# Kernel tuning notes

Hardware: AMD Instinct MI355X
Metric: run time of the kernel (lower is better)

## Reference

```python
import jax, jax.numpy as jnp
import numpy as np

H = 8  # num_heads

def setup_inputs() -> dict:
    key = jax.random.key(0)
    ks = jax.random.split(key, 10)
    B, N, C = 2048, 50, 256
    x = jax.random.normal(ks[0], (B, N, C), dtype=jnp.float32)
    adj = jax.random.uniform(ks[1], (B, N, N), dtype=jnp.float32)
    matrix = jax.random.normal(ks[2], (B, N, N), dtype=jnp.float32)
    s = 0.02
    Wq = jax.random.normal(ks[3], (C, C), dtype=jnp.float32) * s
    bq = jnp.zeros((C,), dtype=jnp.float32)
    Wk = jax.random.normal(ks[4], (C, C), dtype=jnp.float32) * s
    bk = jnp.zeros((C,), dtype=jnp.float32)
    Wa = jax.random.normal(ks[5], (N * H, N), dtype=jnp.float32) * s
    ba = jnp.zeros((N * H,), dtype=jnp.float32)
    Wm = jax.random.normal(ks[6], (N * H, N), dtype=jnp.float32) * s
    bm = jnp.zeros((N * H,), dtype=jnp.float32)
    lambdas = jnp.tile(jnp.array([[1.0, 0.0, 0.0]], dtype=jnp.float32), (H, 1))
    return {"x": x, "adj": adj, "matrix": matrix, "Wq": Wq, "bq": bq,
            "Wk": Wk, "bk": bk, "Wa": Wa, "ba": ba, "Wm": Wm, "bm": bm,
            "lambdas": lambdas}

def reference(x, adj, matrix, Wq, bq, Wk, bk, Wa, ba, Wm, bm, lambdas):
    B, N, C = x.shape
    D = C // H
    # torch Linear: y = x @ W.T + b
    q = (jnp.einsum('bnc,dc->bnd', x, Wq) + bq).reshape(B, N, H, D).transpose(0, 2, 1, 3)
    k = (jnp.einsum('bnc,dc->bnd', x, Wk) + bk).reshape(B, N, H, D).transpose(0, 2, 1, 3)
    # NOTE: original code computes v with self.k (faithful to source)
    v = k
    # scale uses full dim C (x.shape[-1]), not head_dim, as in source
    attn = jax.nn.softmax(jnp.einsum('bhnd,bhmd->bhnm', q, k) * (C ** -0.5), axis=-1)
    adj_a = jax.nn.softmax(
        (jnp.einsum('bnm,km->bnk', adj, Wa) + ba).reshape(B, N, H, N).transpose(0, 2, 1, 3), axis=-1)
    mat_a = jax.nn.softmax(
        (jnp.einsum('bnm,km->bnk', matrix, Wm) + bm).reshape(B, N, H, N).transpose(0, 2, 1, 3), axis=-1)
    lam = jax.nn.softmax(lambdas, axis=-1)  # [H, 3]
    l0 = lam[:, 0][None, :, None, None]
    l1 = lam[:, 1][None, :, None, None]
    l2 = lam[:, 2][None, :, None, None]
    mix = l0 * attn + l1 * adj_a + l2 * mat_a  # [B, H, N, N]
    out = jnp.einsum('bhnm,bhmd->bhnd', mix, v).transpose(0, 2, 1, 3).reshape(B, N, C)
    return out
```

## Files before the change

kernel.cpp:

```cpp
#include <hip/hip_runtime.h>
#include <stdint.h>


typedef __attribute__((ext_vector_type(8))) short short8;
typedef __attribute__((ext_vector_type(4))) float f32x4;
typedef unsigned short u16;

#define L2E 1.4426950408889634f

__device__ __forceinline__ u16 f2bf(float f) {
  unsigned int u = __float_as_uint(f);
  u = (u + 0x7FFFu + ((u >> 16) & 1u)) >> 16;
  return (u16)u;
}
__device__ __forceinline__ unsigned cvt_pk_bf16(float a, float b) {
  unsigned r;
  asm("v_cvt_pk_bf16_f32 %0, %1, %2" : "=v"(r) : "v"(a), "v"(b));
  return r;
}
__device__ __forceinline__ float exp2_fast(float x) {
#if __has_builtin(__builtin_amdgcn_exp2f)
  return __builtin_amdgcn_exp2f(x);
#else
  return __expf(x * 0.6931471805599453f);
#endif
}
__device__ __forceinline__ void lds_fence() {
  asm volatile("s_waitcnt lgkmcnt(0)" ::: "memory");
}

__global__ __launch_bounds__(256) void cast_all(
    const float* __restrict__ adj, const float* __restrict__ mat,
    const float* __restrict__ Wq, const float* __restrict__ Wk,
    const float* __restrict__ Wa, const float* __restrict__ Wm,
    u16* __restrict__ da, u16* __restrict__ dm, u16* __restrict__ wqk,
    u16* __restrict__ wab, u16* __restrict__ wmb,
    u16* __restrict__ qws, u16* __restrict__ kws) {
  const int blk = blockIdx.x, tid = threadIdx.x;
  if (blk < 2048) {
    const int total8 = (102416 * 64) / 8;
    for (int i8 = blk * 256 + tid; i8 < total8; i8 += 2048 * 256) {
      int r = i8 >> 3, c = (i8 & 7) * 8;
      short8 oa = (short8){0,0,0,0,0,0,0,0};
      short8 om = (short8){0,0,0,0,0,0,0,0};
      if (r < 102400) {
        size_t base = (size_t)r * 50;
#pragma unroll
        for (int p = 0; p < 4; ++p) {
          int col = c + 2 * p;
          if (col < 50) {
            float2 va = *(const float2*)(adj + base + col);
            float2 vm = *(const float2*)(mat + base + col);
            oa[2*p] = f2bf(va.x); oa[2*p+1] = f2bf(va.y);
            om[2*p] = f2bf(vm.x); om[2*p+1] = f2bf(vm.y);
          }
        }
      }
      *(short8*)(da + (size_t)i8 * 8) = oa;
      *(short8*)(dm + (size_t)i8 * 8) = om;
    }
  } else if (blk < 2112) {
    int idx8 = (blk - 2048) * 256 + tid;
    int r = idx8 >> 5, c = (idx8 & 31) * 8;
    const float* src = (r < 256) ? (Wq + (size_t)r * 256 + c)
                                 : (Wk + (size_t)(r - 256) * 256 + c);
    float4 v0 = *(const float4*)(src);
    float4 v1 = *(const float4*)(src + 4);
    short8 o;
    o[0] = f2bf(v0.x); o[1] = f2bf(v0.y); o[2] = f2bf(v0.z); o[3] = f2bf(v0.w);
    o[4] = f2bf(v1.x); o[5] = f2bf(v1.y); o[6] = f2bf(v1.z); o[7] = f2bf(v1.w);
    *(short8*)(wqk + (size_t)idx8 * 8) = o;
  } else if (blk < 2216) {
    int idx = (blk - 2112) * 256 + tid;
    int r = idx >> 6, c = idx & 63;
    float va = 0.f, vm = 0.f;
    if (r < 400 && c < 50) { va = Wa[r * 50 + c]; vm = Wm[r * 50 + c]; }
    wab[idx] = f2bf(va); wmb[idx] = f2bf(vm);
  } else {
    short8 z = (short8){0,0,0,0,0,0,0,0};
    *(short8*)(qws + (size_t)819200 * 32 + tid * 8) = z;
    *(short8*)(kws + (size_t)819200 * 32 + tid * 8) = z;
  }
}

__global__ __launch_bounds__(256) void proj_kernel(
    const float* __restrict__ x, const u16* __restrict__ wqk,
    const float* __restrict__ bq, const float* __restrict__ bk,
    u16* __restrict__ qws, u16* __restrict__ kws) {
  __shared__ char xa[64 * 512];
  __shared__ char wb[64 * 512];
  const int tid = threadIdx.x;
  const int m0 = blockIdx.x * 64;

#pragma unroll
  for (int t = 0; t < 16; ++t) {
    int idx = tid + t * 256;
    int r = idx >> 6, c4 = idx & 63;
    float4 v = *(const float4*)(x + (size_t)(m0 + r) * 256 + c4 * 4);
    unsigned long long pk = (unsigned long long)f2bf(v.x)
                          | ((unsigned long long)f2bf(v.y) << 16)
                          | ((unsigned long long)f2bf(v.z) << 32)
                          | ((unsigned long long)f2bf(v.w) << 48);
    int byte = (r * 512 + c4 * 8) ^ ((r & 7) << 4);
    *(unsigned long long*)(xa + byte) = pk;
  }
  __syncthreads();

  const int w = tid >> 6, l = tid & 63, lo = l & 15, g = l >> 4;
  short8 a[8];
  const int ra = 16 * w + lo;
#pragma unroll
  for (int ks = 0; ks < 8; ++ks)
    a[ks] = *(const short8*)(xa + ((ra * 512 + ks * 64 + g * 16) ^ ((ra & 7) << 4)));
  size_t mb[4];
#pragma unroll
  for (int i = 0; i < 4; ++i) {
    int m = m0 + 16 * w + 4 * g + i;
    int b = m / 50;
    int n = m - 50 * b;
    mb[i] = (size_t)b * 12800 + (size_t)n * 32;
  }

  for (int nt = 0; nt < 8; ++nt) {
    __syncthreads();
#pragma unroll
    for (int t = 0; t < 8; ++t) {
      int idx = tid + t * 256;
      int r = idx >> 5, c8 = idx & 31;
      short8 v = *(const short8*)(wqk + (size_t)(nt * 64 + r) * 256 + c8 * 8);
      int byte = (r * 512 + c8 * 16) ^ ((r & 7) << 4);
      *(short8*)(wb + byte) = v;
    }
    __syncthreads();

    f32x4 acc[4];
#pragma unroll
    for (int tj = 0; tj < 4; ++tj) acc[tj] = (f32x4){0.f, 0.f, 0.f, 0.f};
#pragma unroll
    for (int ks = 0; ks < 8; ++ks) {
#pragma unroll
      for (int tj = 0; tj < 4; ++tj) {
        int rb = 16 * tj + lo;
        short8 bb = *(const short8*)(wb + ((rb * 512 + ks * 64 + g * 16) ^ ((rb & 7) << 4)));
        acc[tj] = __builtin_amdgcn_mfma_f32_16x16x32_bf16(a[ks], bb, acc[tj], 0, 0, 0);
      }
    }
    const int n0 = nt * 64;
#pragma unroll
    for (int tj = 0; tj < 4; ++tj) {
      int j = n0 + 16 * tj + lo;
      int jj = j & 255;
      float bias = (j < 256) ? bq[jj] : bk[jj];
      u16* dst = (j < 256) ? qws : kws;
      int hh = jj >> 5, d = jj & 31;
#pragma unroll
      for (int i = 0; i < 4; ++i)
        dst[mb[i] + (size_t)hh * 1600 + d] = f2bf(acc[tj][i] + bias);
    }
  }
}

__device__ __forceinline__ void sm_pv_tile(
    f32x4 (&S)[4], const float (&bml)[4][4], float sl2e, float lam,
    u16* pb, const short8 (&vb)[2][2], f32x4 (&Otj)[2], int tj, int lo, int g) {
  float p[4][4];
#pragma unroll
  for (int ti = 0; ti < 4; ++ti)
#pragma unroll
    for (int i = 0; i < 4; ++i)
      p[ti][i] = exp2_fast(S[ti][i] * sl2e + bml[ti][i]);
  float t0 = (p[0][0] + p[0][1]) + (p[0][2] + p[0][3]);
  float t1 = (p[1][0] + p[1][1]) + (p[1][2] + p[1][3]);
  float t2 = (p[2][0] + p[2][1]) + (p[2][2] + p[2][3]);
  float t3 = (p[3][0] + p[3][1]) + (p[3][2] + p[3][3]);
  float sum = (t0 + t1) + (t2 + t3);
  sum += __shfl_xor(sum, 16);
  sum += __shfl_xor(sum, 32);
  float r = lam * __builtin_amdgcn_rcpf(sum);
  u16* base = pb + (tj & 1) * 1152 + lo * 72;
#pragma unroll
  for (int ti = 0; ti < 4; ++ti) {
    uint2 pk;
    pk.x = cvt_pk_bf16(p[ti][0] * r, p[ti][1] * r);
    pk.y = cvt_pk_bf16(p[ti][2] * r, p[ti][3] * r);
    *(uint2*)(base + 16 * ti + 4 * g) = pk;
  }
  lds_fence();
#pragma unroll
  for (int ks = 0; ks < 2; ++ks) {
    short8 pa = *(const short8*)(pb + (tj & 1) * 1152 + lo * 72 + ks * 32 + g * 8);
#pragma unroll
    for (int tjv = 0; tjv < 2; ++tjv)
      Otj[tjv] = __builtin_amdgcn_mfma_f32_16x16x32_bf16(pa, vb[tjv][ks], Otj[tjv], 0, 0, 0);
  }
}

__device__ __forceinline__ void adj_phase(
    const u16* __restrict__ aBase, const u16* __restrict__ bBase,
    const float* __restrict__ biasPtr, float lam,
    u16* pb, const short8 (&vb)[2][2], f32x4 (&O)[4][2], int lo, int g) {
  short8 af[4][2];
#pragma unroll
  for (int ti = 0; ti < 4; ++ti)
#pragma unroll
    for (int ks = 0; ks < 2; ++ks)
      af[ti][ks] = *(const short8*)(aBase + (size_t)(lo + 16 * ti) * 64 + ks * 32 + g * 8);
  float bml[4][4];
#pragma unroll
  for (int ti = 0; ti < 4; ++ti)
#pragma unroll
    for (int i = 0; i < 4; ++i) {
      int m = 16 * ti + 4 * g + i;
      bml[ti][i] = (m < 50) ? biasPtr[m] * L2E : -1.0e30f;
    }
#pragma unroll
  for (int tj = 0; tj < 4; ++tj) {
    short8 bf0 = *(const short8*)(bBase + (size_t)(lo + 16 * tj) * 64 + g * 8);
    short8 bf1 = *(const short8*)(bBase + (size_t)(lo + 16 * tj) * 64 + 32 + g * 8);
    f32x4 S[4];
#pragma unroll
    for (int ti = 0; ti < 4; ++ti) S[ti] = (f32x4){0.f, 0.f, 0.f, 0.f};
#pragma unroll
    for (int ti = 0; ti < 4; ++ti)
      S[ti] = __builtin_amdgcn_mfma_f32_16x16x32_bf16(af[ti][0], bf0, S[ti], 0, 0, 0);
#pragma unroll
    for (int ti = 0; ti < 4; ++ti)
      S[ti] = __builtin_amdgcn_mfma_f32_16x16x32_bf16(af[ti][1], bf1, S[ti], 0, 0, 0);
    sm_pv_tile(S, bml, L2E, lam, pb, vb, O[tj], tj, lo, g);
  }
}

__global__ __launch_bounds__(256) void attn_kernel(
    const u16* __restrict__ qws, const u16* __restrict__ kws,
    const u16* __restrict__ adjb, const u16* __restrict__ matb,
    const u16* __restrict__ wab, const u16* __restrict__ wmb,
    const float* __restrict__ ba, const float* __restrict__ bm,
    const float* __restrict__ lambdas, float* __restrict__ out) {
  __shared__ u16 smem[4][2304];
  const int tid = threadIdx.x;
  const int w = tid >> 6, l = tid & 63, lo = l & 15, g = l >> 4;
  const int bh = blockIdx.x * 4 + w;
  const int b = bh >> 3, h = bh & 7;
  u16* sh = smem[w];

  float la = lambdas[h * 3 + 0], lb = lambdas[h * 3 + 1], lc = lambdas[h * 3 + 2];
  float lmx = fmaxf(la, fmaxf(lb, lc));
  float e0 = __expf(la - lmx), e1 = __expf(lb - lmx), e2 = __expf(lc - lmx);
  float einv = 1.f / (e0 + e1 + e2);
  float lam0 = e0 * einv, lam1 = e1 * einv, lam2 = e2 * einv;

  {
    const u16* kr = kws + (size_t)bh * 1600 + (size_t)l * 32;
#pragma unroll
    for (int ch = 0; ch < 4; ++ch) {
      short8 v = (short8){0, 0, 0, 0, 0, 0, 0, 0};
      if (l < 50) v = *(const short8*)(kr + ch * 8);
#pragma unroll
      for (int jj = 0; jj < 8; ++jj)
        sh[(ch * 8 + jj) * 72 + l] = (u16)v[jj];
    }
  }
  lds_fence();
  short8 vb[2][2];
#pragma unroll
  for (int tjv = 0; tjv < 2; ++tjv)
#pragma unroll
    for (int ks = 0; ks < 2; ++ks)
      vb[tjv][ks] = *(const short8*)(sh + (lo + 16 * tjv) * 72 + ks * 32 + g * 8);

  f32x4 O[4][2];
#pragma unroll
  for (int ti = 0; ti < 4; ++ti)
#pragma unroll
    for (int tjv = 0; tjv < 2; ++tjv) O[ti][tjv] = (f32x4){0.f, 0.f, 0.f, 0.f};

  {
    short8 af[4];
#pragma unroll
    for (int ti = 0; ti < 4; ++ti)
      af[ti] = *(const short8*)(kws + (size_t)bh * 1600 + (size_t)(lo + 16 * ti) * 32 + g * 8);
    float bml[4][4];
#pragma unroll
    for (int ti = 0; ti < 4; ++ti)
#pragma unroll
      for (int i = 0; i < 4; ++i)
        bml[ti][i] = (16 * ti + 4 * g + i < 50) ? 0.f : -1.0e30f;
#pragma unroll
    for (int tj = 0; tj < 4; ++tj) {
      short8 qf = *(const short8*)(qws + (size_t)bh * 1600 + (size_t)(lo + 16 * tj) * 32 + g * 8);
      f32x4 S[4];
#pragma unroll
      for (int ti = 0; ti < 4; ++ti) S[ti] = (f32x4){0.f, 0.f, 0.f, 0.f};
#pragma unroll
      for (int ti = 0; ti < 4; ++ti)
        S[ti] = __builtin_amdgcn_mfma_f32_16x16x32_bf16(af[ti], qf, S[ti], 0, 0, 0);
      sm_pv_tile(S, bml, 0.0625f * L2E, lam0, sh, vb, O[tj], tj, lo, g);
    }
  }
  adj_phase(wab + (size_t)h * 3200, adjb + (size_t)b * 3200, ba + h * 50,
            lam1, sh, vb, O, lo, g);
  adj_phase(wmb + (size_t)h * 3200, matb + (size_t)b * 3200, bm + h * 50,
            lam2, sh, vb, O, lo, g);

  float* ob = out + ((size_t)b * 50) * 256 + h * 32;
#pragma unroll
  for (int ti = 0; ti < 4; ++ti)
#pragma unroll
    for (int i = 0; i < 4; ++i) {
      int n = 16 * ti + 4 * g + i;
      if (n < 50) {
#pragma unroll
        for (int tjv = 0; tjv < 2; ++tjv)
          ob[(size_t)n * 256 + 16 * tjv + lo] = O[ti][tjv][i];
      }
    }
}

extern "C" void kernel_launch(void* const* d_in, const int* in_sizes, int n_in,
                              void* d_out, int out_size, void* d_ws, size_t ws_size,
                              hipStream_t stream) {
  const float* x       = (const float*)d_in[0];
  const float* adj     = (const float*)d_in[1];
  const float* mat     = (const float*)d_in[2];
  const float* Wq      = (const float*)d_in[3];
  const float* bq      = (const float*)d_in[4];
  const float* Wk      = (const float*)d_in[5];
  const float* bk      = (const float*)d_in[6];
  const float* Wa      = (const float*)d_in[7];
  const float* ba      = (const float*)d_in[8];
  const float* Wm      = (const float*)d_in[9];
  const float* bm      = (const float*)d_in[10];
  const float* lambdas = (const float*)d_in[11];
  float* out = (float*)d_out;

  char* ws = (char*)d_ws;
  u16* wqk  = (u16*)ws; ws += (size_t)512 * 256 * 2;
  u16* wab  = (u16*)ws; ws += (size_t)416 * 64 * 2;
  u16* wmb  = (u16*)ws; ws += (size_t)416 * 64 * 2;
  u16* adjb = (u16*)ws; ws += (size_t)102416 * 64 * 2;
  u16* matb = (u16*)ws; ws += (size_t)102416 * 64 * 2;
  u16* qws  = (u16*)ws; ws += (size_t)819264 * 32 * 2;
  u16* kws  = (u16*)ws; ws += (size_t)819264 * 32 * 2;

  cast_all<<<2217, 256, 0, stream>>>(adj, mat, Wq, Wk, Wa, Wm,
                                     adjb, matb, wqk, wab, wmb, qws, kws);
  proj_kernel<<<1600, 256, 0, stream>>>(x, wqk, bq, bk, qws, kws);
  attn_kernel<<<4096, 256, 0, stream>>>(qws, kws, adjb, matb, wab, wmb, ba, bm, lambdas, out);
}
```

Before: 203.9 us.

## Fuse adj/matrix bf16 cast into attention kernel via swizzled LDS staging

```diff
diff --git a/kernel.cpp b/kernel.cpp
--- a/kernel.cpp
+++ b/kernel.cpp
@@ -26,41 +26,19 @@
 #endif
 }
 __device__ __forceinline__ void lds_fence() {
-  asm volatile("s_waitcnt lgkmcnt(0)" ::: "memory");
+  asm volatile("s_waitcnt lgkmcnt(0)");
 }
 
 __global__ __launch_bounds__(256) void cast_all(
-    const float* __restrict__ adj, const float* __restrict__ mat,
     const float* __restrict__ Wq, const float* __restrict__ Wk,
     const float* __restrict__ Wa, const float* __restrict__ Wm,
-    u16* __restrict__ da, u16* __restrict__ dm, u16* __restrict__ wqk,
-    u16* __restrict__ wab, u16* __restrict__ wmb,
+    const float* __restrict__ ba, const float* __restrict__ bm,
+    u16* __restrict__ wqk, u16* __restrict__ wab, u16* __restrict__ wmb,
+    float* __restrict__ bap, float* __restrict__ bmp,
     u16* __restrict__ qws, u16* __restrict__ kws) {
   const int blk = blockIdx.x, tid = threadIdx.x;
-  if (blk < 2048) {
-    const int total8 = (102416 * 64) / 8;
-    for (int i8 = blk * 256 + tid; i8 < total8; i8 += 2048 * 256) {
-      int r = i8 >> 3, c = (i8 & 7) * 8;
-      short8 oa = (short8){0,0,0,0,0,0,0,0};
-      short8 om = (short8){0,0,0,0,0,0,0,0};
-      if (r < 102400) {
-        size_t base = (size_t)r * 50;
-#pragma unroll
-        for (int p = 0; p < 4; ++p) {
-          int col = c + 2 * p;
-          if (col < 50) {
-            float2 va = *(const float2*)(adj + base + col);
-            float2 vm = *(const float2*)(mat + base + col);
-            oa[2*p] = f2bf(va.x); oa[2*p+1] = f2bf(va.y);
-            om[2*p] = f2bf(vm.x); om[2*p+1] = f2bf(vm.y);
-          }
-        }
-      }
-      *(short8*)(da + (size_t)i8 * 8) = oa;
-      *(short8*)(dm + (size_t)i8 * 8) = om;
-    }
-  } else if (blk < 2112) {
-    int idx8 = (blk - 2048) * 256 + tid;
+  if (blk < 64) {
+    int idx8 = blk * 256 + tid;
     int r = idx8 >> 5, c = (idx8 & 31) * 8;
     const float* src = (r < 256) ? (Wq + (size_t)r * 256 + c)
                                  : (Wk + (size_t)(r - 256) * 256 + c);
@@ -70,8 +48,8 @@
     o[0] = f2bf(v0.x); o[1] = f2bf(v0.y); o[2] = f2bf(v0.z); o[3] = f2bf(v0.w);
     o[4] = f2bf(v1.x); o[5] = f2bf(v1.y); o[6] = f2bf(v1.z); o[7] = f2bf(v1.w);
     *(short8*)(wqk + (size_t)idx8 * 8) = o;
-  } else if (blk < 2216) {
-    int idx = (blk - 2112) * 256 + tid;
+  } else if (blk < 168) {
+    int idx = (blk - 64) * 256 + tid;
     int r = idx >> 6, c = idx & 63;
     float va = 0.f, vm = 0.f;
     if (r < 400 && c < 50) { va = Wa[r * 50 + c]; vm = Wm[r * 50 + c]; }
@@ -80,6 +58,13 @@
     short8 z = (short8){0,0,0,0,0,0,0,0};
     *(short8*)(qws + (size_t)819200 * 32 + tid * 8) = z;
     *(short8*)(kws + (size_t)819200 * 32 + tid * 8) = z;
+#pragma unroll
+    for (int j = 0; j < 2; ++j) {
+      int idx = tid + 256 * j;
+      int hh = idx >> 6, m = idx & 63;
+      bap[idx] = (m < 50) ? ba[hh * 50 + m] : 0.f;
+      bmp[idx] = (m < 50) ? bm[hh * 50 + m] : 0.f;
+    }
   }
 }
 
@@ -158,6 +143,11 @@
         dst[mb[i] + (size_t)hh * 1600 + d] = f2bf(acc[tj][i] + bias);
     }
   }
+}
+
+__device__ __forceinline__ short8 ldsfrag(const u16* bLds, int row, int ks, int g) {
+  return *(const short8*)((const char*)bLds +
+         (((row) * 128 + ks * 64 + g * 16) ^ (((row) & 7) << 4)));
 }
 
 __device__ __forceinline__ void sm_pv_tile(
@@ -196,9 +186,8 @@
 }
 
 __device__ __forceinline__ void adj_phase(
-    const u16* __restrict__ aBase, const u16* __restrict__ bBase,
-    const float* __restrict__ biasPtr, float lam,
-    u16* pb, const short8 (&vb)[2][2], f32x4 (&O)[4][2], int lo, int g) {
+    const u16* __restrict__ aBase, const u16* bLds, const float* __restrict__ bPad,
+    float lam, u16* pb, const short8 (&vb)[2][2], f32x4 (&O)[4][2], int lo, int g) {
   short8 af[4][2];
 #pragma unroll
   for (int ti = 0; ti < 4; ++ti)
@@ -207,42 +196,70 @@
       af[ti][ks] = *(const short8*)(aBase + (size_t)(lo + 16 * ti) * 64 + ks * 32 + g * 8);
   float bml[4][4];
 #pragma unroll
-  for (int ti = 0; ti < 4; ++ti)
-#pragma unroll
-    for (int i = 0; i < 4; ++i) {
-      int m = 16 * ti + 4 * g + i;
-      bml[ti][i] = (m < 50) ? biasPtr[m] * L2E : -1.0e30f;
-    }
+  for (int ti = 0; ti < 4; ++ti) {
+    f32x4 bv = *(const f32x4*)(bPad + 16 * ti + 4 * g);
+#pragma unroll
+    for (int i = 0; i < 4; ++i)
+      bml[ti][i] = (16 * ti + 4 * g + i < 50) ? bv[i] * L2E : -1.0e30f;
+  }
+  short8 bc0 = ldsfrag(bLds, lo, 0, g);
+  short8 bc1 = ldsfrag(bLds, lo, 1, g);
 #pragma unroll
   for (int tj = 0; tj < 4; ++tj) {
-    short8 bf0 = *(const short8*)(bBase + (size_t)(lo + 16 * tj) * 64 + g * 8);
-    short8 bf1 = *(const short8*)(bBase + (size_t)(lo + 16 * tj) * 64 + 32 + g * 8);
+    short8 bn0, bn1;
+    if (tj < 3) {
+      bn0 = ldsfrag(bLds, lo + 16 * (tj + 1), 0, g);
+      bn1 = ldsfrag(bLds, lo + 16 * (tj + 1), 1, g);
+    }
     f32x4 S[4];
 #pragma unroll
     for (int ti = 0; ti < 4; ++ti) S[ti] = (f32x4){0.f, 0.f, 0.f, 0.f};
 #pragma unroll
     for (int ti = 0; ti < 4; ++ti)
-      S[ti] = __builtin_amdgcn_mfma_f32_16x16x32_bf16(af[ti][0], bf0, S[ti], 0, 0, 0);
+      S[ti] = __builtin_amdgcn_mfma_f32_16x16x32_bf16(af[ti][0], bc0, S[ti], 0, 0, 0);
 #pragma unroll
     for (int ti = 0; ti < 4; ++ti)
-      S[ti] = __builtin_amdgcn_mfma_f32_16x16x32_bf16(af[ti][1], bf1, S[ti], 0, 0, 0);
+      S[ti] = __builtin_amdgcn_mfma_f32_16x16x32_bf16(af[ti][1], bc1, S[ti], 0, 0, 0);
     sm_pv_tile(S, bml, L2E, lam, pb, vb, O[tj], tj, lo, g);
+    bc0 = bn0; bc1 = bn1;
   }
 }
 
 __global__ __launch_bounds__(256) void attn_kernel(
     const u16* __restrict__ qws, const u16* __restrict__ kws,
-    const u16* __restrict__ adjb, const u16* __restrict__ matb,
+    const float* __restrict__ adjf, const float* __restrict__ matf,
     const u16* __restrict__ wab, const u16* __restrict__ wmb,
-    const float* __restrict__ ba, const float* __restrict__ bm,
+    const float* __restrict__ bap, const float* __restrict__ bmp,
     const float* __restrict__ lambdas, float* __restrict__ out) {
   __shared__ u16 smem[4][2304];
+  __shared__ u16 adjm[2][4096];
   const int tid = threadIdx.x;
   const int w = tid >> 6, l = tid & 63, lo = l & 15, g = l >> 4;
   const int bh = blockIdx.x * 4 + w;
   const int b = bh >> 3, h = bh & 7;
   u16* sh = smem[w];
 
+  {
+    const float* s0 = adjf + (size_t)b * 2500;
+    const float* s1 = matf + (size_t)b * 2500;
+#pragma unroll
+    for (int mtx = 0; mtx < 2; ++mtx) {
+      const float* s = mtx ? s1 : s0;
+      unsigned* dstm = (unsigned*)adjm[mtx];
+#pragma unroll
+      for (int t = 0; t < 8; ++t) {
+        int word = tid + t * 256;
+        int r = word >> 5, c2 = word & 31;
+        unsigned val = 0;
+        if (r < 50 && c2 < 25) {
+          float2 v = *(const float2*)(s + r * 50 + c2 * 2);
+          val = cvt_pk_bf16(v.x, v.y);
+        }
+        dstm[word ^ ((r & 7) << 2)] = val;
+      }
+    }
+  }
+
   float la = lambdas[h * 3 + 0], lb = lambdas[h * 3 + 1], lc = lambdas[h * 3 + 2];
   float lmx = fmaxf(la, fmaxf(lb, lc));
   float e0 = __expf(la - lmx), e1 = __expf(lb - lmx), e2 = __expf(lc - lmx);
@@ -285,22 +302,26 @@
 #pragma unroll
       for (int i = 0; i < 4; ++i)
         bml[ti][i] = (16 * ti + 4 * g + i < 50) ? 0.f : -1.0e30f;
+    const u16* qbase = qws + (size_t)bh * 1600;
+    short8 qc = *(const short8*)(qbase + (size_t)lo * 32 + g * 8);
 #pragma unroll
     for (int tj = 0; tj < 4; ++tj) {
-      short8 qf = *(const short8*)(qws + (size_t)bh * 1600 + (size_t)(lo + 16 * tj) * 32 + g * 8);
+      short8 qn;
+      if (tj < 3)
+        qn = *(const short8*)(qbase + (size_t)(lo + 16 * (tj + 1)) * 32 + g * 8);
       f32x4 S[4];
 #pragma unroll
       for (int ti = 0; ti < 4; ++ti) S[ti] = (f32x4){0.f, 0.f, 0.f, 0.f};
 #pragma unroll
       for (int ti = 0; ti < 4; ++ti)
-        S[ti] = __builtin_amdgcn_mfma_f32_16x16x32_bf16(af[ti], qf, S[ti], 0, 0, 0);
+        S[ti] = __builtin_amdgcn_mfma_f32_16x16x32_bf16(af[ti], qc, S[ti], 0, 0, 0);
       sm_pv_tile(S, bml, 0.0625f * L2E, lam0, sh, vb, O[tj], tj, lo, g);
-    }
-  }
-  adj_phase(wab + (size_t)h * 3200, adjb + (size_t)b * 3200, ba + h * 50,
-            lam1, sh, vb, O, lo, g);
-  adj_phase(wmb + (size_t)h * 3200, matb + (size_t)b * 3200, bm + h * 50,
-            lam2, sh, vb, O, lo, g);
+      qc = qn;
+    }
+  }
+  __syncthreads();
+  adj_phase(wab + (size_t)h * 3200, adjm[0], bap + h * 64, lam1, sh, vb, O, lo, g);
+  adj_phase(wmb + (size_t)h * 3200, adjm[1], bmp + h * 64, lam2, sh, vb, O, lo, g);
 
   float* ob = out + ((size_t)b * 50) * 256 + h * 32;
 #pragma unroll
@@ -334,16 +355,17 @@
   float* out = (float*)d_out;
 
   char* ws = (char*)d_ws;
-  u16* wqk  = (u16*)ws; ws += (size_t)512 * 256 * 2;
-  u16* wab  = (u16*)ws; ws += (size_t)416 * 64 * 2;
-  u16* wmb  = (u16*)ws; ws += (size_t)416 * 64 * 2;
-  u16* adjb = (u16*)ws; ws += (size_t)102416 * 64 * 2;
-  u16* matb = (u16*)ws; ws += (size_t)102416 * 64 * 2;
-  u16* qws  = (u16*)ws; ws += (size_t)819264 * 32 * 2;
-  u16* kws  = (u16*)ws; ws += (size_t)819264 * 32 * 2;
-
-  cast_all<<<2217, 256, 0, stream>>>(adj, mat, Wq, Wk, Wa, Wm,
-                                     adjb, matb, wqk, wab, wmb, qws, kws);
+  u16* wqk   = (u16*)ws; ws += (size_t)512 * 256 * 2;
+  u16* wab   = (u16*)ws; ws += (size_t)416 * 64 * 2;
+  u16* wmb   = (u16*)ws; ws += (size_t)416 * 64 * 2;
+  float* bap = (float*)ws; ws += (size_t)512 * 4;
+  float* bmp = (float*)ws; ws += (size_t)512 * 4;
+  u16* qws   = (u16*)ws; ws += (size_t)819264 * 32 * 2;
+  u16* kws   = (u16*)ws; ws += (size_t)819264 * 32 * 2;
+
+  cast_all<<<169, 256, 0, stream>>>(Wq, Wk, Wa, Wm, ba, bm,
+                                    wqk, wab, wmb, bap, bmp, qws, kws);
   proj_kernel<<<1600, 256, 0, stream>>>(x, wqk, bq, bk, qws, kws);
-  attn_kernel<<<4096, 256, 0, stream>>>(qws, kws, adjb, matb, wab, wmb, ba, bm, lambdas, out);
-}
+  attn_kernel<<<4096, 256, 0, stream>>>(qws, kws, adj, mat, wab, wmb,
+                                        bap, bmp, lambdas, out);
+}
```

New measurement: 228.7 us. 12.2% more time.

## Split each (batch, head) attention across two waves and precompute padded biases

Applied to the files above, without the earlier changes.

```diff
diff --git a/kernel.cpp b/kernel.cpp
--- a/kernel.cpp
+++ b/kernel.cpp
@@ -26,15 +26,17 @@
 #endif
 }
 __device__ __forceinline__ void lds_fence() {
-  asm volatile("s_waitcnt lgkmcnt(0)" ::: "memory");
+  asm volatile("s_waitcnt lgkmcnt(0)");
 }
 
 __global__ __launch_bounds__(256) void cast_all(
     const float* __restrict__ adj, const float* __restrict__ mat,
     const float* __restrict__ Wq, const float* __restrict__ Wk,
     const float* __restrict__ Wa, const float* __restrict__ Wm,
+    const float* __restrict__ ba, const float* __restrict__ bm,
     u16* __restrict__ da, u16* __restrict__ dm, u16* __restrict__ wqk,
     u16* __restrict__ wab, u16* __restrict__ wmb,
+    float* __restrict__ bap, float* __restrict__ bmp, float* __restrict__ maskv,
     u16* __restrict__ qws, u16* __restrict__ kws) {
   const int blk = blockIdx.x, tid = threadIdx.x;
   if (blk < 2048) {
@@ -80,6 +82,14 @@
     short8 z = (short8){0,0,0,0,0,0,0,0};
     *(short8*)(qws + (size_t)819200 * 32 + tid * 8) = z;
     *(short8*)(kws + (size_t)819200 * 32 + tid * 8) = z;
+#pragma unroll
+    for (int j = 0; j < 2; ++j) {
+      int idx = tid + 256 * j;
+      int hh = idx >> 6, m = idx & 63;
+      bap[idx] = (m < 50) ? ba[hh * 50 + m] * L2E : -1.0e30f;
+      bmp[idx] = (m < 50) ? bm[hh * 50 + m] * L2E : -1.0e30f;
+    }
+    if (tid < 64) maskv[tid] = (tid < 50) ? 0.f : -1.0e30f;
   }
 }
 
@@ -160,9 +170,10 @@
   }
 }
 
+
 __device__ __forceinline__ void sm_pv_tile(
-    f32x4 (&S)[4], const float (&bml)[4][4], float sl2e, float lam,
-    u16* pb, const short8 (&vb)[2][2], f32x4 (&Otj)[2], int tj, int lo, int g) {
+    f32x4 (&S)[4], const f32x4 (&bml)[4], float sl2e, float lam,
+    u16* pb, const short8 (&vb)[2][2], f32x4 (&Otj)[2], int buf, int lo, int g) {
   float p[4][4];
 #pragma unroll
   for (int ti = 0; ti < 4; ++ti)
@@ -177,7 +188,7 @@
   sum += __shfl_xor(sum, 16);
   sum += __shfl_xor(sum, 32);
   float r = lam * __builtin_amdgcn_rcpf(sum);
-  u16* base = pb + (tj & 1) * 1152 + lo * 72;
+  u16* base = pb + buf * 1152 + lo * 72;
 #pragma unroll
   for (int ti = 0; ti < 4; ++ti) {
     uint2 pk;
@@ -188,7 +199,7 @@
   lds_fence();
 #pragma unroll
   for (int ks = 0; ks < 2; ++ks) {
-    short8 pa = *(const short8*)(pb + (tj & 1) * 1152 + lo * 72 + ks * 32 + g * 8);
+    short8 pa = *(const short8*)(pb + buf * 1152 + lo * 72 + ks * 32 + g * 8);
 #pragma unroll
     for (int tjv = 0; tjv < 2; ++tjv)
       Otj[tjv] = __builtin_amdgcn_mfma_f32_16x16x32_bf16(pa, vb[tjv][ks], Otj[tjv], 0, 0, 0);
@@ -197,36 +208,38 @@
 
 __device__ __forceinline__ void adj_phase(
     const u16* __restrict__ aBase, const u16* __restrict__ bBase,
-    const float* __restrict__ biasPtr, float lam,
-    u16* pb, const short8 (&vb)[2][2], f32x4 (&O)[4][2], int lo, int g) {
+    const float* __restrict__ bPad, float lam,
+    u16* pb, const short8 (&vb)[2][2], f32x4 (&O)[2][2], int half, int lo, int g) {
   short8 af[4][2];
 #pragma unroll
   for (int ti = 0; ti < 4; ++ti)
 #pragma unroll
     for (int ks = 0; ks < 2; ++ks)
       af[ti][ks] = *(const short8*)(aBase + (size_t)(lo + 16 * ti) * 64 + ks * 32 + g * 8);
-  float bml[4][4];
+  short8 bf[2][2];
+#pragma unroll
+  for (int tjl = 0; tjl < 2; ++tjl) {
+    int n = lo + 16 * (2 * half + tjl);
+#pragma unroll
+    for (int ks = 0; ks < 2; ++ks)
+      bf[tjl][ks] = *(const short8*)(bBase + (size_t)n * 64 + ks * 32 + g * 8);
+  }
+  f32x4 bml[4];
 #pragma unroll
   for (int ti = 0; ti < 4; ++ti)
-#pragma unroll
-    for (int i = 0; i < 4; ++i) {
-      int m = 16 * ti + 4 * g + i;
-      bml[ti][i] = (m < 50) ? biasPtr[m] * L2E : -1.0e30f;
-    }
-#pragma unroll
-  for (int tj = 0; tj < 4; ++tj) {
-    short8 bf0 = *(const short8*)(bBase + (size_t)(lo + 16 * tj) * 64 + g * 8);
-    short8 bf1 = *(const short8*)(bBase + (size_t)(lo + 16 * tj) * 64 + 32 + g * 8);
+    bml[ti] = *(const f32x4*)(bPad + 16 * ti + 4 * g);
+#pragma unroll
+  for (int tjl = 0; tjl < 2; ++tjl) {
     f32x4 S[4];
 #pragma unroll
     for (int ti = 0; ti < 4; ++ti) S[ti] = (f32x4){0.f, 0.f, 0.f, 0.f};
 #pragma unroll
     for (int ti = 0; ti < 4; ++ti)
-      S[ti] = __builtin_amdgcn_mfma_f32_16x16x32_bf16(af[ti][0], bf0, S[ti], 0, 0, 0);
+      S[ti] = __builtin_amdgcn_mfma_f32_16x16x32_bf16(af[ti][0], bf[tjl][0], S[ti], 0, 0, 0);
 #pragma unroll
     for (int ti = 0; ti < 4; ++ti)
-      S[ti] = __builtin_amdgcn_mfma_f32_16x16x32_bf16(af[ti][1], bf1, S[ti], 0, 0, 0);
-    sm_pv_tile(S, bml, L2E, lam, pb, vb, O[tj], tj, lo, g);
+      S[ti] = __builtin_amdgcn_mfma_f32_16x16x32_bf16(af[ti][1], bf[tjl][1], S[ti], 0, 0, 0);
+    sm_pv_tile(S, bml, L2E, lam, pb, vb, O[tjl], tjl, lo, g);
   }
 }
 
@@ -234,12 +247,14 @@
     const u16* __restrict__ qws, const u16* __restrict__ kws,
     const u16* __restrict__ adjb, const u16* __restrict__ matb,
     const u16* __restrict__ wab, const u16* __restrict__ wmb,
-    const float* __restrict__ ba, const float* __restrict__ bm,
+    const float* __restrict__ bap, const float* __restrict__ bmp,
+    const float* __restrict__ maskv,
     const float* __restrict__ lambdas, float* __restrict__ out) {
   __shared__ u16 smem[4][2304];
   const int tid = threadIdx.x;
   const int w = tid >> 6, l = tid & 63, lo = l & 15, g = l >> 4;
-  const int bh = blockIdx.x * 4 + w;
+  const int bh = blockIdx.x * 2 + (w >> 1);
+  const int half = w & 1;
   const int b = bh >> 3, h = bh & 7;
   u16* sh = smem[w];
 
@@ -268,52 +283,56 @@
     for (int ks = 0; ks < 2; ++ks)
       vb[tjv][ks] = *(const short8*)(sh + (lo + 16 * tjv) * 72 + ks * 32 + g * 8);
 
-  f32x4 O[4][2];
-#pragma unroll
-  for (int ti = 0; ti < 4; ++ti)
-#pragma unroll
-    for (int tjv = 0; tjv < 2; ++tjv) O[ti][tjv] = (f32x4){0.f, 0.f, 0.f, 0.f};
+  f32x4 O[2][2];
+#pragma unroll
+  for (int tjl = 0; tjl < 2; ++tjl)
+#pragma unroll
+    for (int tjv = 0; tjv < 2; ++tjv) O[tjl][tjv] = (f32x4){0.f, 0.f, 0.f, 0.f};
 
   {
     short8 af[4];
 #pragma unroll
     for (int ti = 0; ti < 4; ++ti)
       af[ti] = *(const short8*)(kws + (size_t)bh * 1600 + (size_t)(lo + 16 * ti) * 32 + g * 8);
-    float bml[4][4];
+    short8 qf[2];
+#pragma unroll
+    for (int tjl = 0; tjl < 2; ++tjl)
+      qf[tjl] = *(const short8*)(qws + (size_t)bh * 1600 +
+                                 (size_t)(lo + 16 * (2 * half + tjl)) * 32 + g * 8);
+    f32x4 bml[4];
 #pragma unroll
     for (int ti = 0; ti < 4; ++ti)
-#pragma unroll
-      for (int i = 0; i < 4; ++i)
-        bml[ti][i] = (16 * ti + 4 * g + i < 50) ? 0.f : -1.0e30f;
-#pragma unroll
-    for (int tj = 0; tj < 4; ++tj) {
-      short8 qf = *(const short8*)(qws + (size_t)bh * 1600 + (size_t)(lo + 16 * tj) * 32 + g * 8);
+      bml[ti] = *(const f32x4*)(maskv + 16 * ti + 4 * g);
+#pragma unroll
+    for (int tjl = 0; tjl < 2; ++tjl) {
       f32x4 S[4];
 #pragma unroll
       for (int ti = 0; ti < 4; ++ti) S[ti] = (f32x4){0.f, 0.f, 0.f, 0.f};
 #pragma unroll
       for (int ti = 0; ti < 4; ++ti)
-        S[ti] = __builtin_amdgcn_mfma_f32_16x16x32_bf16(af[ti], qf, S[ti], 0, 0, 0);
-      sm_pv_tile(S, bml, 0.0625f * L2E, lam0, sh, vb, O[tj], tj, lo, g);
-    }
-  }
-  adj_phase(wab + (size_t)h * 3200, adjb + (size_t)b * 3200, ba + h * 50,
-            lam1, sh, vb, O, lo, g);
-  adj_phase(wmb + (size_t)h * 3200, matb + (size_t)b * 3200, bm + h * 50,
-            lam2, sh, vb, O, lo, g);
-
-  float* ob = out + ((size_t)b * 50) * 256 + h * 32;
-#pragma unroll
-  for (int ti = 0; ti < 4; ++ti)
+        S[ti] = __builtin_amdgcn_mfma_f32_16x16x32_bf16(af[ti], qf[tjl], S[ti], 0, 0, 0);
+      sm_pv_tile(S, bml, 0.0625f * L2E, lam0, sh, vb, O[tjl], tjl, lo, g);
+    }
+  }
+  adj_phase(wab + (size_t)h * 3200, adjb + (size_t)b * 3200, bap + h * 64,
+            lam1, sh, vb, O, half, lo, g);
+  adj_phase(wmb + (size_t)h * 3200, matb + (size_t)b * 3200, bmp + h * 64,
+            lam2, sh, vb, O, half, lo, g);
+
+  float* ob = out + (size_t)b * 12800 + h * 32;
+#pragma unroll
+  for (int tjl = 0; tjl < 2; ++tjl) {
+    int tj = 2 * half + tjl;
 #pragma unroll
     for (int i = 0; i < 4; ++i) {
-      int n = 16 * ti + 4 * g + i;
+      int n = 16 * tj + 4 * g + i;
       if (n < 50) {
 #pragma unroll
         for (int tjv = 0; tjv < 2; ++tjv)
-          ob[(size_t)n * 256 + 16 * tjv + lo] = O[ti][tjv][i];
+          ob[(size_t)n * 256 + 16 * tjv + lo] = O[tjl][tjv][i];
       }
     }
+  }
 }
 
 extern "C" void kernel_launch(void* const* d_in, const int* in_sizes, int n_in,
@@ -334,16 +353,21 @@
   float* out = (float*)d_out;
 
   char* ws = (char*)d_ws;
-  u16* wqk  = (u16*)ws; ws += (size_t)512 * 256 * 2;
-  u16* wab  = (u16*)ws; ws += (size_t)416 * 64 * 2;
-  u16* wmb  = (u16*)ws; ws += (size_t)416 * 64 * 2;
-  u16* adjb = (u16*)ws; ws += (size_t)102416 * 64 * 2;
-  u16* matb = (u16*)ws; ws += (size_t)102416 * 64 * 2;
-  u16* qws  = (u16*)ws; ws += (size_t)819264 * 32 * 2;
-  u16* kws  = (u16*)ws; ws += (size_t)819264 * 32 * 2;
-
-  cast_all<<<2217, 256, 0, stream>>>(adj, mat, Wq, Wk, Wa, Wm,
-                                     adjb, matb, wqk, wab, wmb, qws, kws);
+  u16* wqk    = (u16*)ws; ws += (size_t)512 * 256 * 2;
+  u16* wab    = (u16*)ws; ws += (size_t)416 * 64 * 2;
+  u16* wmb    = (u16*)ws; ws += (size_t)416 * 64 * 2;
+  float* bap  = (float*)ws; ws += (size_t)512 * 4;
+  float* bmp  = (float*)ws; ws += (size_t)512 * 4;
+  float* mskv = (float*)ws; ws += (size_t)64 * 4;
+  u16* adjb   = (u16*)ws; ws += (size_t)102416 * 64 * 2;
+  u16* matb   = (u16*)ws; ws += (size_t)102416 * 64 * 2;
+  u16* qws    = (u16*)ws; ws += (size_t)819264 * 32 * 2;
+  u16* kws    = (u16*)ws; ws += (size_t)819264 * 32 * 2;
+
+  cast_all<<<2217, 256, 0, stream>>>(adj, mat, Wq, Wk, Wa, Wm, ba, bm,
+                                     adjb, matb, wqk, wab, wmb,
+                                     bap, bmp, mskv, qws, kws);
   proj_kernel<<<1600, 256, 0, stream>>>(x, wqk, bq, bk, qws, kws);
-  attn_kernel<<<4096, 256, 0, stream>>>(qws, kws, adjb, matb, wab, wmb, ba, bm, lambdas, out);
-}
+  attn_kernel<<<8192, 256, 0, stream>>>(qws, kws, adjb, matb, wab, wmb,
+                                        bap, bmp, mskv, lambdas, out);
+}
```

New measurement: 233.6 us. +14.6%, slower.
